# Kernel tuning notes

Hardware: AMD Instinct MI355X
Metric: run time of the kernel (lower is better)

## Reference

```python
import jax, jax.numpy as jnp
import numpy as np

B, IN, H = 32768, 256, 256
CONCAT = IN + H

def _xavier(key, shape):
    fan_in, fan_out = shape
    limit = float(np.sqrt(6.0 / (fan_in + fan_out)))
    return jax.random.uniform(key, shape, jnp.float32, -limit, limit)

def setup_inputs() -> dict:
    key = jax.random.key(0)
    k = jax.random.split(key, 6)
    return {
        "x": jax.random.normal(k[0], (B, 1, IN), jnp.float32),
        "h_prev": jax.random.normal(k[1], (B, 1, H), jnp.float32),
        "wr": _xavier(k[2], (CONCAT, H)),
        "wz": _xavier(k[3], (CONCAT, H)),
        "whh": _xavier(k[4], (H, H)),
        "whx": _xavier(k[5], (IN, H)),
        "br": jnp.zeros((H,), jnp.float32),
        "bz": jnp.zeros((H,), jnp.float32),
        "bh": jnp.zeros((H,), jnp.float32),
    }

def reference(x, h_prev, wr, wz, whh, whx, br, bz, bh):
    # x: [B,1,IN], h_prev: [B,1,H]
    xc = jnp.concatenate([x, h_prev], axis=2)                  # [B,1,IN+H]
    r = jax.nn.sigmoid(jnp.matmul(xc, wr) + br)                # reset gate
    z = jax.nn.sigmoid(jnp.matmul(xc, wz) + bz)                # update gate
    g = jnp.tanh(jnp.matmul(r * h_prev, whh) + jnp.matmul(x, whx) + bh)
    h = (1 - z) * h_prev + z * g                               # gated blend
    return h
```

## Files before the change

kernel.cpp:

```cpp
#include <hip/hip_runtime.h>
#include <hip/hip_bf16.h>
#include <stdint.h>


typedef float  f32x4  __attribute__((ext_vector_type(4)));
typedef __bf16 bf16x8 __attribute__((ext_vector_type(8)));
typedef short  s16x8  __attribute__((ext_vector_type(8)));

#define B_TOT   32768
#define MT      64
#define WRZ_ELEMS (512*512)
#define WG_ELEMS  (256*512)

__device__ __forceinline__ unsigned short f2b(float f) {
    union { float f; unsigned int u; } v; v.f = f;
    unsigned int r = (v.u + 0x7FFFu + ((v.u >> 16) & 1u)) >> 16;
    return (unsigned short)r;
}
__device__ __forceinline__ float b2f(unsigned short b) {
    union { unsigned int u; float f; } v; v.u = ((unsigned int)b) << 16;
    return v.f;
}
__device__ __forceinline__ float sigmoid_f(float x) {
    return 1.0f / (1.0f + __expf(-x));
}
__device__ __forceinline__ float tanh_f(float x) {
    return 1.0f - 2.0f / (__expf(2.0f * x) + 1.0f);
}

__device__ __forceinline__ int lds_idx(int row, int col) {
    return row * 512 + ((((col >> 3) ^ (row & 7)) << 3) | (col & 7));
}

__global__ void prep_weights(const float* __restrict__ wr,
                             const float* __restrict__ wz,
                             const float* __restrict__ whh,
                             const float* __restrict__ whx,
                             unsigned short* __restrict__ wrz,
                             unsigned short* __restrict__ wg) {
    const int b = blockIdx.x;
    const int t = threadIdx.x;
    union { s16x8 v; unsigned short u[8]; } tmp;

    if (b < 128) {
        int w = b >> 4, ks = b & 15;
        int jn = t >> 6, l = t & 63;
        int kbase = ks * 32 + ((l >> 4) << 3);
        int n = 32 * w + ((jn & 1) << 4) + (l & 15);
        const float* src = (jn < 2) ? wr : wz;
        #pragma unroll
        for (int jj = 0; jj < 8; ++jj)
            tmp.u[jj] = f2b(src[(kbase + jj) * 256 + n]);
        *reinterpret_cast<s16x8*>(wrz + (size_t)w * 32768 + ks * 2048 + t * 8) = tmp.v;
    } else {
        int b2 = b - 128;
        int w = b2 >> 3, ksp = b2 & 7;
        int ksl = t >> 7, j = (t >> 6) & 1, l = t & 63;
        int ks = ksp * 2 + ksl;
        int kbase = ks * 32 + ((l >> 4) << 3);
        int n = 32 * w + (j << 4) + (l & 15);
        #pragma unroll
        for (int jj = 0; jj < 8; ++jj) {
            int k = kbase + jj;
            tmp.u[jj] = f2b((k < 256) ? whx[k * 256 + n] : whh[(k - 256) * 256 + n]);
        }
        *reinterpret_cast<s16x8*>(wg + (size_t)w * 16384 + ksp * 2048 + t * 8) = tmp.v;
    }
}

__global__ __launch_bounds__(512, 3)
void gru_fused(const float* __restrict__ x, const float* __restrict__ h,
               const unsigned short* __restrict__ wrz,
               const unsigned short* __restrict__ wg,
               const float* __restrict__ br, const float* __restrict__ bz,
               const float* __restrict__ bh, float* __restrict__ out) {
    __shared__ unsigned short xcA[64 * 512];

    const int tid  = threadIdx.x;
    const int lane = tid & 63;
    const int wv   = tid >> 6;
    const int m0   = lane & 15;
    const int q    = lane >> 4;
    const int rowBase = blockIdx.x * MT;

    float brv[2], bzv[2], bhv[2];
    #pragma unroll
    for (int j = 0; j < 2; ++j) {
        int col = 32 * wv + j * 16 + m0;
        brv[j] = br[col]; bzv[j] = bz[col]; bhv[j] = bh[col];
    }

    #pragma unroll
    for (int it = 0; it < 8; ++it) {
        int row = it * 8 + wv;
        size_t g = (size_t)(rowBase + row) * 256 + lane * 4;
        float4 xv = *reinterpret_cast<const float4*>(x + g);
        float4 hv = *reinterpret_cast<const float4*>(h + g);
        ushort4 xb, hb;
        xb.x = f2b(xv.x); xb.y = f2b(xv.y); xb.z = f2b(xv.z); xb.w = f2b(xv.w);
        hb.x = f2b(hv.x); hb.y = f2b(hv.y); hb.z = f2b(hv.z); hb.w = f2b(hv.w);
        *reinterpret_cast<ushort4*>(&xcA[lds_idx(row, lane * 4)])       = xb;
        *reinterpret_cast<ushort4*>(&xcA[lds_idx(row, 256 + lane * 4)]) = hb;
    }

    const unsigned short* wrzP = wrz + (size_t)wv * 32768;
    const unsigned short* wgP  = wg  + (size_t)wv * 16384;

    s16x8 bR[4], nR[4];
    #pragma unroll
    for (int jn = 0; jn < 4; ++jn)
        bR[jn] = *reinterpret_cast<const s16x8*>(wrzP + jn * 512 + lane * 8);

    __syncthreads();

    f32x4 rz[4][4];
    f32x4 gac[2][4];
    #pragma unroll
    for (int jn = 0; jn < 4; ++jn)
        #pragma unroll
        for (int mt = 0; mt < 4; ++mt)
            rz[jn][mt] = (f32x4){0.f, 0.f, 0.f, 0.f};
    #pragma unroll
    for (int j = 0; j < 2; ++j)
        #pragma unroll
        for (int mt = 0; mt < 4; ++mt)
            gac[j][mt] = (f32x4){0.f, 0.f, 0.f, 0.f};

    for (int ks = 0; ks < 8; ++ks) {
        bf16x8 afr[4];
        #pragma unroll
        for (int mt = 0; mt < 4; ++mt) {
            s16x8 raw = *reinterpret_cast<const s16x8*>(
                &xcA[lds_idx(mt * 16 + m0, ks * 32 + q * 8)]);
            afr[mt] = __builtin_bit_cast(bf16x8, raw);
        }
        #pragma unroll
        for (int jn = 0; jn < 4; ++jn)
            nR[jn] = *reinterpret_cast<const s16x8*>(
                wrzP + (ks + 1) * 2048 + jn * 512 + lane * 8);
        s16x8 bG0 = *reinterpret_cast<const s16x8*>(wgP + ks * 1024 + lane * 8);
        s16x8 bG1 = *reinterpret_cast<const s16x8*>(wgP + ks * 1024 + 512 + lane * 8);
        #pragma unroll
        for (int jn = 0; jn < 4; ++jn) {
            bf16x8 bfr = __builtin_bit_cast(bf16x8, bR[jn]);
            #pragma unroll
            for (int mt = 0; mt < 4; ++mt)
                rz[jn][mt] = __builtin_amdgcn_mfma_f32_16x16x32_bf16(
                    afr[mt], bfr, rz[jn][mt], 0, 0, 0);
        }
        {
            bf16x8 g0 = __builtin_bit_cast(bf16x8, bG0);
            bf16x8 g1 = __builtin_bit_cast(bf16x8, bG1);
            #pragma unroll
            for (int mt = 0; mt < 4; ++mt)
                gac[0][mt] = __builtin_amdgcn_mfma_f32_16x16x32_bf16(
                    afr[mt], g0, gac[0][mt], 0, 0, 0);
            #pragma unroll
            for (int mt = 0; mt < 4; ++mt)
                gac[1][mt] = __builtin_amdgcn_mfma_f32_16x16x32_bf16(
                    afr[mt], g1, gac[1][mt], 0, 0, 0);
        }
        #pragma unroll
        for (int jn = 0; jn < 4; ++jn) bR[jn] = nR[jn];
    }
    for (int ks = 8; ks < 16; ++ks) {
        bf16x8 afr[4];
        #pragma unroll
        for (int mt = 0; mt < 4; ++mt) {
            s16x8 raw = *reinterpret_cast<const s16x8*>(
                &xcA[lds_idx(mt * 16 + m0, ks * 32 + q * 8)]);
            afr[mt] = __builtin_bit_cast(bf16x8, raw);
        }
        int ksn = (ks + 1) & 15;
        #pragma unroll
        for (int jn = 0; jn < 4; ++jn)
            nR[jn] = *reinterpret_cast<const s16x8*>(
                wrzP + ksn * 2048 + jn * 512 + lane * 8);
        #pragma unroll
        for (int jn = 0; jn < 4; ++jn) {
            bf16x8 bfr = __builtin_bit_cast(bf16x8, bR[jn]);
            #pragma unroll
            for (int mt = 0; mt < 4; ++mt)
                rz[jn][mt] = __builtin_amdgcn_mfma_f32_16x16x32_bf16(
                    afr[mt], bfr, rz[jn][mt], 0, 0, 0);
        }
        #pragma unroll
        for (int jn = 0; jn < 4; ++jn) bR[jn] = nR[jn];
    }
    __syncthreads();

    s16x8 tG[2], nT[2];
    #pragma unroll
    for (int j = 0; j < 2; ++j)
        tG[j] = *reinterpret_cast<const s16x8*>(
            wgP + 8 * 1024 + j * 512 + lane * 8);

    #pragma unroll
    for (int j = 0; j < 2; ++j) {
        int col = 32 * wv + j * 16 + m0;
        #pragma unroll
        for (int mt = 0; mt < 4; ++mt) {
            #pragma unroll
            for (int rg = 0; rg < 4; ++rg) {
                int row = mt * 16 + q * 4 + rg;
                float hval = b2f(xcA[lds_idx(row, 256 + col)]);
                float rs = sigmoid_f(rz[j][mt][rg] + brv[j]);
                xcA[lds_idx(row, col)] = f2b(rs * hval);
                rz[j][mt][rg] = hval;
            }
        }
    }
    __syncthreads();

    for (int kt = 0; kt < 8; ++kt) {
        bf16x8 afr[4];
        #pragma unroll
        for (int mt = 0; mt < 4; ++mt) {
            s16x8 raw = *reinterpret_cast<const s16x8*>(
                &xcA[lds_idx(mt * 16 + m0, kt * 32 + q * 8)]);
            afr[mt] = __builtin_bit_cast(bf16x8, raw);
        }
        int ktn = 8 + ((kt + 1) & 7);
        #pragma unroll
        for (int j = 0; j < 2; ++j)
            nT[j] = *reinterpret_cast<const s16x8*>(
                wgP + ktn * 1024 + j * 512 + lane * 8);
        #pragma unroll
        for (int j = 0; j < 2; ++j) {
            bf16x8 bfr = __builtin_bit_cast(bf16x8, tG[j]);
            #pragma unroll
            for (int mt = 0; mt < 4; ++mt)
                gac[j][mt] = __builtin_amdgcn_mfma_f32_16x16x32_bf16(
                    afr[mt], bfr, gac[j][mt], 0, 0, 0);
        }
        #pragma unroll
        for (int j = 0; j < 2; ++j) tG[j] = nT[j];
    }

    #pragma unroll
    for (int j = 0; j < 2; ++j) {
        int col = 32 * wv + j * 16 + m0;
        #pragma unroll
        for (int mt = 0; mt < 4; ++mt) {
            #pragma unroll
            for (int rg = 0; rg < 4; ++rg) {
                int row = mt * 16 + q * 4 + rg;
                float zs = sigmoid_f(rz[2 + j][mt][rg] + bzv[j]);
                float gv = tanh_f(gac[j][mt][rg] + bhv[j]);
                float hval = rz[j][mt][rg];
                out[(size_t)(rowBase + row) * 256 + col] = hval + zs * (gv - hval);
            }
        }
    }
}

extern "C" void kernel_launch(void* const* d_in, const int* in_sizes, int n_in,
                              void* d_out, int out_size, void* d_ws, size_t ws_size,
                              hipStream_t stream) {
    const float* x   = (const float*)d_in[0];
    const float* h   = (const float*)d_in[1];
    const float* wr  = (const float*)d_in[2];
    const float* wz  = (const float*)d_in[3];
    const float* whh = (const float*)d_in[4];
    const float* whx = (const float*)d_in[5];
    const float* br  = (const float*)d_in[6];
    const float* bz  = (const float*)d_in[7];
    const float* bh  = (const float*)d_in[8];
    float* out = (float*)d_out;

    unsigned short* wrz = (unsigned short*)d_ws;
    unsigned short* wg  = wrz + WRZ_ELEMS;

    prep_weights<<<192, 256, 0, stream>>>(wr, wz, whh, whx, wrz, wg);
    gru_fused<<<B_TOT / MT, 512, 0, stream>>>(x, h, wrz, wg, br, bz, bh, out);
}
```

Baseline: 156.1 us.

## Deepen weight prefetch to two k-steps per group and fully unroll GEMM loops

Restructures the GEMM main loops so weight fragments for two k-steps (both the rz and gate weights) are prefetched one group ahead into a double-buffered register array, and fully unrolls these loops. Launch bounds drop from 3 to 2 waves-per-EU occupancy to give the compiler room for the larger register footprint. The input conversion to bf16 now uses a packed two-element intrinsic. The aim is to hide global weight-load latency behind more MFMA work, at the cost of lower occupancy and higher register pressure.

```diff
diff --git a/kernel.cpp b/kernel.cpp
--- a/kernel.cpp
+++ b/kernel.cpp
@@ -20,6 +20,10 @@
 __device__ __forceinline__ float b2f(unsigned short b) {
     union { unsigned int u; float f; } v; v.u = ((unsigned int)b) << 16;
     return v.f;
+}
+__device__ __forceinline__ ushort2 pk2(float a, float b) {
+    __hip_bfloat162 t = __float22bfloat162_rn(make_float2(a, b));
+    union { __hip_bfloat162 h; ushort2 u; } c; c.h = t; return c.u;
 }
 __device__ __forceinline__ float sigmoid_f(float x) {
     return 1.0f / (1.0f + __expf(-x));
@@ -68,7 +72,7 @@
     }
 }
 
-__global__ __launch_bounds__(512, 3)
+__global__ __launch_bounds__(512, 2)
 void gru_fused(const float* __restrict__ x, const float* __restrict__ h,
                const unsigned short* __restrict__ wrz,
                const unsigned short* __restrict__ wg,
@@ -96,9 +100,10 @@
         size_t g = (size_t)(rowBase + row) * 256 + lane * 4;
         float4 xv = *reinterpret_cast<const float4*>(x + g);
         float4 hv = *reinterpret_cast<const float4*>(h + g);
-        ushort4 xb, hb;
-        xb.x = f2b(xv.x); xb.y = f2b(xv.y); xb.z = f2b(xv.z); xb.w = f2b(xv.w);
-        hb.x = f2b(hv.x); hb.y = f2b(hv.y); hb.z = f2b(hv.z); hb.w = f2b(hv.w);
+        ushort2 x0 = pk2(xv.x, xv.y), x1 = pk2(xv.z, xv.w);
+        ushort2 h0 = pk2(hv.x, hv.y), h1 = pk2(hv.z, hv.w);
+        ushort4 xb = make_ushort4(x0.x, x0.y, x1.x, x1.y);
+        ushort4 hb = make_ushort4(h0.x, h0.y, h1.x, h1.y);
         *reinterpret_cast<ushort4*>(&xcA[lds_idx(row, lane * 4)])       = xb;
         *reinterpret_cast<ushort4*>(&xcA[lds_idx(row, 256 + lane * 4)]) = hb;
     }
@@ -106,10 +111,18 @@
     const unsigned short* wrzP = wrz + (size_t)wv * 32768;
     const unsigned short* wgP  = wg  + (size_t)wv * 16384;
 
-    s16x8 bR[4], nR[4];
-    #pragma unroll
-    for (int jn = 0; jn < 4; ++jn)
-        bR[jn] = *reinterpret_cast<const s16x8*>(wrzP + jn * 512 + lane * 8);
+    s16x8 Bb[2][12];
+    #pragma unroll
+    for (int k2 = 0; k2 < 2; ++k2) {
+        #pragma unroll
+        for (int jn = 0; jn < 4; ++jn)
+            Bb[0][k2 * 6 + jn] = *reinterpret_cast<const s16x8*>(
+                wrzP + k2 * 2048 + jn * 512 + lane * 8);
+        #pragma unroll
+        for (int j = 0; j < 2; ++j)
+            Bb[0][k2 * 6 + 4 + j] = *reinterpret_cast<const s16x8*>(
+                wgP + k2 * 1024 + j * 512 + lane * 8);
+    }
 
     __syncthreads();
 
@@ -126,74 +139,66 @@
         for (int mt = 0; mt < 4; ++mt)
             gac[j][mt] = (f32x4){0.f, 0.f, 0.f, 0.f};
 
-    for (int ks = 0; ks < 8; ++ks) {
-        bf16x8 afr[4];
-        #pragma unroll
-        for (int mt = 0; mt < 4; ++mt) {
-            s16x8 raw = *reinterpret_cast<const s16x8*>(
-                &xcA[lds_idx(mt * 16 + m0, ks * 32 + q * 8)]);
-            afr[mt] = __builtin_bit_cast(bf16x8, raw);
-        }
-        #pragma unroll
-        for (int jn = 0; jn < 4; ++jn)
-            nR[jn] = *reinterpret_cast<const s16x8*>(
-                wrzP + (ks + 1) * 2048 + jn * 512 + lane * 8);
-        s16x8 bG0 = *reinterpret_cast<const s16x8*>(wgP + ks * 1024 + lane * 8);
-        s16x8 bG1 = *reinterpret_cast<const s16x8*>(wgP + ks * 1024 + 512 + lane * 8);
-        #pragma unroll
-        for (int jn = 0; jn < 4; ++jn) {
-            bf16x8 bfr = __builtin_bit_cast(bf16x8, bR[jn]);
-            #pragma unroll
-            for (int mt = 0; mt < 4; ++mt)
-                rz[jn][mt] = __builtin_amdgcn_mfma_f32_16x16x32_bf16(
-                    afr[mt], bfr, rz[jn][mt], 0, 0, 0);
-        }
-        {
-            bf16x8 g0 = __builtin_bit_cast(bf16x8, bG0);
-            bf16x8 g1 = __builtin_bit_cast(bf16x8, bG1);
-            #pragma unroll
-            for (int mt = 0; mt < 4; ++mt)
-                gac[0][mt] = __builtin_amdgcn_mfma_f32_16x16x32_bf16(
-                    afr[mt], g0, gac[0][mt], 0, 0, 0);
-            #pragma unroll
-            for (int mt = 0; mt < 4; ++mt)
-                gac[1][mt] = __builtin_amdgcn_mfma_f32_16x16x32_bf16(
-                    afr[mt], g1, gac[1][mt], 0, 0, 0);
-        }
-        #pragma unroll
-        for (int jn = 0; jn < 4; ++jn) bR[jn] = nR[jn];
-    }
-    for (int ks = 8; ks < 16; ++ks) {
-        bf16x8 afr[4];
-        #pragma unroll
-        for (int mt = 0; mt < 4; ++mt) {
-            s16x8 raw = *reinterpret_cast<const s16x8*>(
-                &xcA[lds_idx(mt * 16 + m0, ks * 32 + q * 8)]);
-            afr[mt] = __builtin_bit_cast(bf16x8, raw);
-        }
-        int ksn = (ks + 1) & 15;
-        #pragma unroll
-        for (int jn = 0; jn < 4; ++jn)
-            nR[jn] = *reinterpret_cast<const s16x8*>(
-                wrzP + ksn * 2048 + jn * 512 + lane * 8);
-        #pragma unroll
-        for (int jn = 0; jn < 4; ++jn) {
-            bf16x8 bfr = __builtin_bit_cast(bf16x8, bR[jn]);
-            #pragma unroll
-            for (int mt = 0; mt < 4; ++mt)
-                rz[jn][mt] = __builtin_amdgcn_mfma_f32_16x16x32_bf16(
-                    afr[mt], bfr, rz[jn][mt], 0, 0, 0);
-        }
-        #pragma unroll
-        for (int jn = 0; jn < 4; ++jn) bR[jn] = nR[jn];
+    #pragma unroll
+    for (int grp = 0; grp < 8; ++grp) {
+        const int cur = grp & 1, nxt = cur ^ 1;
+        if (grp < 7) {
+            int gn = grp + 1;
+            #pragma unroll
+            for (int k2 = 0; k2 < 2; ++k2) {
+                int ks = gn * 2 + k2;
+                #pragma unroll
+                for (int jn = 0; jn < 4; ++jn)
+                    Bb[nxt][k2 * 6 + jn] = *reinterpret_cast<const s16x8*>(
+                        wrzP + ks * 2048 + jn * 512 + lane * 8);
+                if (gn < 4) {
+                    #pragma unroll
+                    for (int j = 0; j < 2; ++j)
+                        Bb[nxt][k2 * 6 + 4 + j] = *reinterpret_cast<const s16x8*>(
+                            wgP + ks * 1024 + j * 512 + lane * 8);
+                }
+            }
+        }
+        #pragma unroll
+        for (int k2 = 0; k2 < 2; ++k2) {
+            int ks = grp * 2 + k2;
+            bf16x8 afr[4];
+            #pragma unroll
+            for (int mt = 0; mt < 4; ++mt) {
+                int row = mt * 16 + m0;
+                int idx = row * 512 + ((((ks << 2) | q) ^ (row & 7)) << 3);
+                afr[mt] = __builtin_bit_cast(bf16x8,
+                    *reinterpret_cast<const s16x8*>(&xcA[idx]));
+            }
+            #pragma unroll
+            for (int jn = 0; jn < 4; ++jn) {
+                bf16x8 bf = __builtin_bit_cast(bf16x8, Bb[cur][k2 * 6 + jn]);
+                #pragma unroll
+                for (int mt = 0; mt < 4; ++mt)
+                    rz[jn][mt] = __builtin_amdgcn_mfma_f32_16x16x32_bf16(
+                        afr[mt], bf, rz[jn][mt], 0, 0, 0);
+            }
+            if (grp < 4) {
+                #pragma unroll
+                for (int j = 0; j < 2; ++j) {
+                    bf16x8 bf = __builtin_bit_cast(bf16x8, Bb[cur][k2 * 6 + 4 + j]);
+                    #pragma unroll
+                    for (int mt = 0; mt < 4; ++mt)
+                        gac[j][mt] = __builtin_amdgcn_mfma_f32_16x16x32_bf16(
+                            afr[mt], bf, gac[j][mt], 0, 0, 0);
+                }
+            }
+        }
     }
     __syncthreads();
 
-    s16x8 tG[2], nT[2];
-    #pragma unroll
-    for (int j = 0; j < 2; ++j)
-        tG[j] = *reinterpret_cast<const s16x8*>(
-            wgP + 8 * 1024 + j * 512 + lane * 8);
+    s16x8 Tb[2][4];
+    #pragma unroll
+    for (int k2 = 0; k2 < 2; ++k2)
+        #pragma unroll
+        for (int j = 0; j < 2; ++j)
+            Tb[0][k2 * 2 + j] = *reinterpret_cast<const s16x8*>(
+                wgP + (8 + k2) * 1024 + j * 512 + lane * 8);
 
     #pragma unroll
     for (int j = 0; j < 2; ++j) {
@@ -212,29 +217,37 @@
     }
     __syncthreads();
 
-    for (int kt = 0; kt < 8; ++kt) {
-        bf16x8 afr[4];
-        #pragma unroll
-        for (int mt = 0; mt < 4; ++mt) {
-            s16x8 raw = *reinterpret_cast<const s16x8*>(
-                &xcA[lds_idx(mt * 16 + m0, kt * 32 + q * 8)]);
-            afr[mt] = __builtin_bit_cast(bf16x8, raw);
-        }
-        int ktn = 8 + ((kt + 1) & 7);
-        #pragma unroll
-        for (int j = 0; j < 2; ++j)
-            nT[j] = *reinterpret_cast<const s16x8*>(
-                wgP + ktn * 1024 + j * 512 + lane * 8);
-        #pragma unroll
-        for (int j = 0; j < 2; ++j) {
-            bf16x8 bfr = __builtin_bit_cast(bf16x8, tG[j]);
-            #pragma unroll
-            for (int mt = 0; mt < 4; ++mt)
-                gac[j][mt] = __builtin_amdgcn_mfma_f32_16x16x32_bf16(
-                    afr[mt], bfr, gac[j][mt], 0, 0, 0);
-        }
-        #pragma unroll
-        for (int j = 0; j < 2; ++j) tG[j] = nT[j];
+    #pragma unroll
+    for (int tg = 0; tg < 4; ++tg) {
+        const int cur = tg & 1, nxt = cur ^ 1;
+        if (tg < 3) {
+            #pragma unroll
+            for (int k2 = 0; k2 < 2; ++k2)
+                #pragma unroll
+                for (int j = 0; j < 2; ++j)
+                    Tb[nxt][k2 * 2 + j] = *reinterpret_cast<const s16x8*>(
+                        wgP + (10 + tg * 2 + k2) * 1024 + j * 512 + lane * 8);
+        }
+        #pragma unroll
+        for (int k2 = 0; k2 < 2; ++k2) {
+            int kt = tg * 2 + k2;
+            bf16x8 afr[4];
+            #pragma unroll
+            for (int mt = 0; mt < 4; ++mt) {
+                int row = mt * 16 + m0;
+                int idx = row * 512 + ((((kt << 2) | q) ^ (row & 7)) << 3);
+                afr[mt] = __builtin_bit_cast(bf16x8,
+                    *reinterpret_cast<const s16x8*>(&xcA[idx]));
+            }
+            #pragma unroll
+            for (int j = 0; j < 2; ++j) {
+                bf16x8 bf = __builtin_bit_cast(bf16x8, Tb[cur][k2 * 2 + j]);
+                #pragma unroll
+                for (int mt = 0; mt < 4; ++mt)
+                    gac[j][mt] = __builtin_amdgcn_mfma_f32_16x16x32_bf16(
+                        afr[mt], bf, gac[j][mt], 0, 0, 0);
+            }
+        }
     }
 
     #pragma unroll
```

Result: no change. 156.0 us (-0.0%).
